# Kernel optimization log

Measured on AMD Instinct MI355X. Metric: run time of the kernel, lower is better.

The kernel has to match this reference:

```python
import jax, jax.numpy as jnp
import numpy as np

N = 50000        # nodes
E = 800000       # edges
F_IN = 128       # dataset.num_features (== dim*heads so all conv layers share in_channels)
DIM = 32         # mParams['dim']
HEADS = 4        # mParams['num_heads']
HC = DIM * HEADS # 128
DEPTH = 2        # mParams['c_depth'] -> total conv layers = DEPTH + 1 = 3
L = DEPTH + 1
DIM2 = 16        # ceil(DIM/2)
NCLS = 6
SLOPE = 0.2      # GATv2Conv default negative_slope


def setup_inputs() -> dict:
    key = jax.random.key(0)
    ks = jax.random.split(key, 20)
    def lin(k, fan_in, shape):
        return jax.random.normal(k, shape, dtype=jnp.float32) / np.sqrt(fan_in)
    x = jax.random.normal(ks[0], (N, F_IN), dtype=jnp.float32)
    edge_index = jax.random.randint(ks[1], (2, E), 0, N, dtype=jnp.int64)
    batch = jnp.zeros((N,), dtype=jnp.int64)
    # stacked GATv2Conv params (all layers have in_channels = 128)
    Wl = lin(ks[2], F_IN, (L, F_IN, HC))   # lin_l weight (source transform)
    Wr = lin(ks[3], F_IN, (L, F_IN, HC))   # lin_r weight (target transform)
    bl = jnp.zeros((L, HC), dtype=jnp.float32)
    br = jnp.zeros((L, HC), dtype=jnp.float32)
    att = lin(ks[4], DIM, (L, HEADS, DIM)) # attention vector a
    cb = jnp.zeros((L, HC), dtype=jnp.float32)  # conv output bias
    W1 = lin(ks[5], HC, (HC, DIM));   b1 = jnp.zeros((DIM,), jnp.float32)
    W2 = lin(ks[6], DIM, (DIM, DIM2)); b2 = jnp.zeros((DIM2,), jnp.float32)
    W3 = lin(ks[7], 2 * DIM2, (2 * DIM2, NCLS)); b3 = jnp.zeros((NCLS,), jnp.float32)
    return {"x": x, "edge_index": edge_index, "batch": batch,
            "Wl": Wl, "Wr": Wr, "bl": bl, "br": br, "att": att, "cb": cb,
            "W1": W1, "b1": b1, "W2": W2, "b2": b2, "W3": W3, "b3": b3}


def _gatv2_layer(h, src, dst, Wl, Wr, bl, br, att, cb):
    # h: [N, F]; src/dst: [Ea] (self-loops included)
    xl = (h @ Wl + bl).reshape(N, HEADS, DIM)  # source-side transform
    xr = (h @ Wr + br).reshape(N, HEADS, DIM)  # target-side transform
    msg = xl[src] + xr[dst]                    # [Ea, H, C]
    e = jnp.where(msg > 0, msg, SLOPE * msg)   # leaky_relu
    score = jnp.einsum('ehc,hc->eh', e, att)   # [Ea, H]
    # scatter-softmax over destination nodes
    m = jax.ops.segment_max(score, dst, num_segments=N)        # [N, H]
    ex = jnp.exp(score - m[dst])
    s = jax.ops.segment_sum(ex, dst, num_segments=N)           # [N, H]
    alpha = ex / (s[dst] + 1e-16)                              # [Ea, H]
    out = jax.ops.segment_sum(alpha[:, :, None] * xl[src], dst, num_segments=N)
    return out.reshape(N, HC) + cb


def reference(x, edge_index, batch, Wl, Wr, bl, br, att, cb, W1, b1, W2, b2, W3, b3):
    src0, dst0 = edge_index[0], edge_index[1]
    loop = jnp.arange(N, dtype=edge_index.dtype)
    src = jnp.concatenate([src0, loop])  # GATv2Conv add_self_loops=True
    dst = jnp.concatenate([dst0, loop])
    h = x
    for i in range(L):
        h = jax.nn.relu(_gatv2_layer(h, src, dst, Wl[i], Wr[i], bl[i], br[i], att[i], cb[i]))
    h = jax.nn.relu(h @ W1 + b1)
    h = jax.nn.relu(h @ W2 + b2)
    # dropout(p=0.5) is identity in eval mode
    e = jnp.concatenate([h[src0], h[dst0]], axis=1)  # [E, 2*DIM2]
    out = e @ W3 + b3                                # [E, NCLS]
    return (out, e)
```

## Files before the change

kernel.cpp:

```cpp
#include <hip/hip_runtime.h>
#include <hip/hip_bf16.h>

typedef __hip_bfloat16 bf16;
typedef __attribute__((ext_vector_type(8))) short bf16x8;
typedef __attribute__((ext_vector_type(4))) float f32x4;

#define N_NODES 50000
#define E_EDGES 800000
#define EA (E_EDGES + N_NODES)
#define HC 128
#define HEADS 4
#define DIM 32
#define DIM2 16
#define NCLS 6
#define SLOPE 0.2f
#define NCHUNK ((N_NODES + 1023) / 1024)
#define XN (N_NODES * HC)
#define GM 32
#define HSTRIDE 152
#define WSWZ_L 32768

__device__ __forceinline__ float b2f(bf16 v) { return __bfloat162float(v); }
__device__ __forceinline__ unsigned short f2bfu(float f) {
    bf16 b = __float2bfloat16(f);
    return *(unsigned short*)&b;
}

__global__ __launch_bounds__(256) void k_detect(const void* wptr, const void* eptr,
                                                int* __restrict__ flags) {
    __shared__ int sb[256], sn[256];
    int tid = threadIdx.x;
    const unsigned short* w = (const unsigned short*)wptr;
    int badf = 0;
    for (int i = tid; i < 4096; i += 256) {
        unsigned v = w[i];
        unsigned ex = (v >> 7) & 0xFF;
        if (v != 0 && (ex < 90 || ex > 150)) badf++;
    }
    const int* ei = (const int*)eptr;
    int nz = 0;
    for (int i = tid; i < 2048; i += 256) {
        if (ei[2 * i + 1] != 0) nz++;
    }
    sb[tid] = badf; sn[tid] = nz;
    __syncthreads();
    for (int ofs = 128; ofs > 0; ofs >>= 1) {
        if (tid < ofs) { sb[tid] += sb[tid + ofs]; sn[tid] += sn[tid + ofs]; }
        __syncthreads();
    }
    if (tid == 0) {
        flags[0] = (sb[0] > 64) ? 1 : 0;
        flags[1] = (sn[0] < 64) ? 1 : 0;
    }
}

__global__ void k_cvt_all(const void* sx, const void* sWl, const void* sWr,
                          const void* sbl, const void* sbr, const void* satt,
                          const void* scb, const void* sW1, const void* sb1,
                          const void* sW2, const void* sb2, const void* sW3,
                          const void* sb3,
                          float* __restrict__ h, float* __restrict__ prm,
                          const int* __restrict__ flags) {
    int i = blockIdx.x * blockDim.x + threadIdx.x;
    if (i >= XN + 104694) return;
    const void* src; float* dst; int off;
    if (i < XN) { src = sx; dst = h; off = i; }
    else {
        int j = i - XN;
        if      (j < 49152)  { src = sWl;  dst = prm;           off = j; }
        else if (j < 98304)  { src = sWr;  dst = prm + 49152;   off = j - 49152; }
        else if (j < 98688)  { src = sbl;  dst = prm + 98304;   off = j - 98304; }
        else if (j < 99072)  { src = sbr;  dst = prm + 98688;   off = j - 98688; }
        else if (j < 99456)  { src = satt; dst = prm + 99072;   off = j - 99072; }
        else if (j < 99840)  { src = scb;  dst = prm + 99456;   off = j - 99456; }
        else if (j < 103936) { src = sW1;  dst = prm + 99840;   off = j - 99840; }
        else if (j < 103968) { src = sb1;  dst = prm + 103936;  off = j - 103936; }
        else if (j < 104480) { src = sW2;  dst = prm + 103968;  off = j - 103968; }
        else if (j < 104496) { src = sb2;  dst = prm + 104480;  off = j - 104480; }
        else if (j < 104688) { src = sW3;  dst = prm + 104496;  off = j - 104496; }
        else                 { src = sb3;  dst = prm + 104688;  off = j - 104688; }
    }
    float v = flags[0] ? ((const float*)src)[off] : b2f(((const bf16*)src)[off]);
    dst[off] = v;
}

__global__ void k_cvti(const void* __restrict__ src, int* __restrict__ dst, int n,
                       const int* __restrict__ flags) {
    int i = blockIdx.x * blockDim.x + threadIdx.x;
    if (i >= n) return;
    int v;
    if (flags[1]) v = (int)((const long long*)src)[i];
    else          v = ((const int*)src)[i];
    if (v < 0) v = 0;
    if (v >= N_NODES) v = N_NODES - 1;
    dst[i] = v;
}

__global__ void k_wswz(const float* __restrict__ prm, unsigned short* __restrict__ wswz) {
    int i = blockIdx.x * blockDim.x + threadIdx.x;
    if (i >= 3 * WSWZ_L) return;
    int L = i / WSWZ_L;
    int e = i % WSWZ_L;
    int ntile = e >> 11;
    int r2 = e & 2047;
    int ks = r2 >> 9;
    int r3 = r2 & 511;
    int lane = r3 >> 3;
    int j = r3 & 7;
    int col = ntile * 16 + (lane & 15);
    int k = ks * 32 + (lane >> 4) * 8 + j;
    float v;
    if (col < HC) v = prm[L * HC * HC + k * HC + col];
    else          v = prm[49152 + L * HC * HC + k * HC + (col - HC)];
    wswz[i] = f2bfu(v);
}

__global__ void k_zero(int* __restrict__ off, int* __restrict__ fill) {
    int i = blockIdx.x * blockDim.x + threadIdx.x;
    if (i <= N_NODES) off[i] = 0;
    if (i < N_NODES) fill[i] = 0;
}

__global__ void k_hist(const int* __restrict__ eidx, int* __restrict__ off) {
    int e = blockIdx.x * blockDim.x + threadIdx.x;
    if (e >= EA) return;
    int dst = (e < E_EDGES) ? eidx[E_EDGES + e] : (e - E_EDGES);
    atomicAdd(&off[dst], 1);
}

__global__ __launch_bounds__(1024) void k_scan1(int* __restrict__ off, int* __restrict__ part) {
    __shared__ int s[1024];
    int tid = threadIdx.x;
    int i = blockIdx.x * 1024 + tid;
    int v = (i < N_NODES) ? off[i] : 0;
    s[tid] = v;
    __syncthreads();
    for (int o = 1; o < 1024; o <<= 1) {
        int t = (tid >= o) ? s[tid - o] : 0;
        __syncthreads();
        s[tid] += t;
        __syncthreads();
    }
    if (i < N_NODES) off[i] = s[tid] - v;
    if (tid == 1023) part[blockIdx.x] = s[1023];
}

__global__ __launch_bounds__(64) void k_scan2(int* __restrict__ part) {
    int tid = threadIdx.x;
    int v = (tid < NCHUNK) ? part[tid] : 0;
    int orig = v;
    for (int o = 1; o < 64; o <<= 1) {
        int t = __shfl_up(v, o);
        if (tid >= o) v += t;
    }
    if (tid < NCHUNK) part[tid] = v - orig;
}

__global__ __launch_bounds__(1024) void k_scan3(int* __restrict__ off, const int* __restrict__ part) {
    int i = blockIdx.x * 1024 + threadIdx.x;
    if (i < N_NODES) off[i] += part[blockIdx.x];
    if (i == 0) off[N_NODES] = EA;
}

__global__ void k_scatter(const int* __restrict__ eidx, const int* __restrict__ off,
                          int* __restrict__ fill, int* __restrict__ csrsrc) {
    int e = blockIdx.x * blockDim.x + threadIdx.x;
    if (e >= EA) return;
    int src, dst;
    if (e < E_EDGES) { src = eidx[e]; dst = eidx[E_EDGES + e]; }
    else             { src = dst = e - E_EDGES; }
    int pos = off[dst] + atomicAdd(&fill[dst], 1);
    if (pos >= 0 && pos < EA) csrsrc[pos] = src;
}

__global__ __launch_bounds__(256) void k_gemm_mfma(
        const float* __restrict__ h,
        const unsigned short* __restrict__ wswz,
        const float* __restrict__ bl, const float* __restrict__ br,
        unsigned* __restrict__ xlbf, float* __restrict__ xr) {
    __shared__ unsigned short hs[GM * HSTRIDE];
    int tid = threadIdx.x;
    int wave = tid >> 6, lane = tid & 63;
    long row0 = (long)blockIdx.x * GM;

    for (int idx = tid; idx < GM * 64; idx += 256) {
        int r = idx >> 6, cp = idx & 63;
        float v0 = 0.f, v1 = 0.f;
        if (row0 + r < N_NODES) {
            const float2 hv = ((const float2*)(h + (row0 + r) * HC))[cp];
            v0 = hv.x; v1 = hv.y;
        }
        unsigned* dst = (unsigned*)&hs[r * HSTRIDE + cp * 2];
        *dst = (unsigned)f2bfu(v0) | ((unsigned)f2bfu(v1) << 16);
    }
    __syncthreads();

    int q = lane >> 4, l16 = lane & 15;
    for (int nt = 0; nt < 4; nt++) {
        int colbase = wave * 64 + nt * 16;
        int col = colbase + l16;
        int ntile = colbase >> 4;
        f32x4 acc0 = {0.f, 0.f, 0.f, 0.f};
        f32x4 acc1 = {0.f, 0.f, 0.f, 0.f};
#pragma unroll
        for (int ks = 0; ks < 4; ks++) {
            bf16x8 bfrag = *(const bf16x8*)(wswz + (((ntile * 4 + ks) * 64 + lane) << 3));
            bf16x8 a0 = *(const bf16x8*)(hs + l16 * HSTRIDE + ks * 32 + q * 8);
            bf16x8 a1 = *(const bf16x8*)(hs + (16 + l16) * HSTRIDE + ks * 32 + q * 8);
            acc0 = __builtin_amdgcn_mfma_f32_16x16x32_bf16(a0, bfrag, acc0, 0, 0, 0);
            acc1 = __builtin_amdgcn_mfma_f32_16x16x32_bf16(a1, bfrag, acc1, 0, 0, 0);
        }
        if (col < HC) {
            float bias = bl[col];
#pragma unroll
            for (int reg = 0; reg < 4; reg++) {
                float v0 = acc0[reg] + bias;
                float v1 = acc1[reg] + bias;
                float p0 = __shfl_xor(v0, 1);
                float p1 = __shfl_xor(v1, 1);
                if ((lane & 1) == 0) {
                    long n0 = row0 + q * 4 + reg;
                    long n1 = row0 + 16 + q * 4 + reg;
                    unsigned u0 = (unsigned)f2bfu(v0) | ((unsigned)f2bfu(p0) << 16);
                    unsigned u1 = (unsigned)f2bfu(v1) | ((unsigned)f2bfu(p1) << 16);
                    int cp = col >> 1;
                    if (n0 < N_NODES) xlbf[n0 * (HC / 2) + cp] = u0;
                    if (n1 < N_NODES) xlbf[n1 * (HC / 2) + cp] = u1;
                }
            }
        } else {
            int c = col - HC;
            float bias = br[c];
#pragma unroll
            for (int reg = 0; reg < 4; reg++) {
                long n0 = row0 + q * 4 + reg;
                long n1 = row0 + 16 + q * 4 + reg;
                if (n0 < N_NODES) xr[n0 * HC + c] = acc0[reg] + bias;
                if (n1 < N_NODES) xr[n1 * HC + c] = acc1[reg] + bias;
            }
        }
    }
}

__global__ __launch_bounds__(256) void k_attn(
        const unsigned* __restrict__ xlbf, const float* __restrict__ xr,
        const int* __restrict__ off, const int* __restrict__ csrsrc,
        const float* __restrict__ att, const float* __restrict__ cb,
        float* __restrict__ hout) {
    int wave = threadIdx.x >> 6;
    int lane = threadIdx.x & 63;
    int node = blockIdx.x * 4 + wave;
    if (node >= N_NODES) return;
    int grp = lane >> 4;
    int gl  = lane & 15;
    int fb  = gl * 8;
    int head = fb >> 5;

    const float4* xrp = (const float4*)(xr + (long)node * HC + fb);
    float4 xa = xrp[0], xb = xrp[1];
    const float4* ap = (const float4*)(att + head * DIM + (fb & 31));
    float4 aa = ap[0], ab = ap[1];

    int e0 = off[node], e1 = off[node + 1];
    if (e0 < 0) e0 = 0;
    if (e1 > EA) e1 = EA;
    if (e1 <= e0) {
        if (grp == 0) {
            float4 z = make_float4(0.f, 0.f, 0.f, 0.f);
            ((float4*)(hout + (long)node * HC + fb))[0] = z;
            ((float4*)(hout + (long)node * HC + fb))[1] = z;
        }
        return;
    }
    int klast = e1 - 1;

    int k0 = e0 + grp;
    int ka = k0 < klast ? k0 : klast;
    int kb = (k0 + 4) < klast ? (k0 + 4) : klast;
    int sa = csrsrc[ka];
    int sb = csrsrc[kb];
    uint4 u0 = ((const uint4*)(xlbf + (long)sa * (HC / 2)))[gl];
    uint4 u1 = ((const uint4*)(xlbf + (long)sb * (HC / 2)))[gl];

    float m = -1e30f, ssum = 0.f;
    float acc[8];
#pragma unroll
    for (int j = 0; j < 8; j++) acc[j] = 0.f;

    for (int kk = k0; kk < e1; kk += 4) {
        uint4 cur = u0;
        u0 = u1;
        int kp = (kk + 8) < klast ? (kk + 8) : klast;
        int sp = csrsrc[kp];
        u1 = ((const uint4*)(xlbf + (long)sp * (HC / 2)))[gl];

        float x0 = __uint_as_float(cur.x << 16);
        float x1 = __uint_as_float(cur.x & 0xffff0000u);
        float x2 = __uint_as_float(cur.y << 16);
        float x3 = __uint_as_float(cur.y & 0xffff0000u);
        float x4 = __uint_as_float(cur.z << 16);
        float x5 = __uint_as_float(cur.z & 0xffff0000u);
        float x6 = __uint_as_float(cur.w << 16);
        float x7 = __uint_as_float(cur.w & 0xffff0000u);
        float m0 = x0 + xa.x, m1 = x1 + xa.y, m2 = x2 + xa.z, m3 = x3 + xa.w;
        float m4 = x4 + xb.x, m5 = x5 + xb.y, m6 = x6 + xb.z, m7 = x7 + xb.w;
        float l0 = fmaxf(m0, SLOPE * m0), l1 = fmaxf(m1, SLOPE * m1);
        float l2 = fmaxf(m2, SLOPE * m2), l3 = fmaxf(m3, SLOPE * m3);
        float l4 = fmaxf(m4, SLOPE * m4), l5 = fmaxf(m5, SLOPE * m5);
        float l6 = fmaxf(m6, SLOPE * m6), l7 = fmaxf(m7, SLOPE * m7);
        float p = l0 * aa.x + l1 * aa.y + l2 * aa.z + l3 * aa.w
                + l4 * ab.x + l5 * ab.y + l6 * ab.z + l7 * ab.w;
        p += __shfl_xor(p, 1);
        p += __shfl_xor(p, 2);
        float mn = fmaxf(m, p);
        float sc = __expf(m - mn);
        float ex = __expf(p - mn);
        ssum = ssum * sc + ex;
        acc[0] = acc[0] * sc + ex * x0;
        acc[1] = acc[1] * sc + ex * x1;
        acc[2] = acc[2] * sc + ex * x2;
        acc[3] = acc[3] * sc + ex * x3;
        acc[4] = acc[4] * sc + ex * x4;
        acc[5] = acc[5] * sc + ex * x5;
        acc[6] = acc[6] * sc + ex * x6;
        acc[7] = acc[7] * sc + ex * x7;
        m = mn;
    }

#pragma unroll
    for (int d = 16; d <= 32; d <<= 1) {
        float mo = __shfl_xor(m, d);
        float so = __shfl_xor(ssum, d);
        float ao[8];
#pragma unroll
        for (int j = 0; j < 8; j++) ao[j] = __shfl_xor(acc[j], d);
        float mn = fmaxf(m, mo);
        float s1 = __expf(m - mn);
        float s2 = __expf(mo - mn);
        ssum = ssum * s1 + so * s2;
#pragma unroll
        for (int j = 0; j < 8; j++) acc[j] = acc[j] * s1 + ao[j] * s2;
        m = mn;
    }

    if (grp == 0) {
        float inv = 1.f / (ssum + 1e-16f);
        const float4* cbp = (const float4*)(cb + fb);
        float4 c0 = cbp[0], c1 = cbp[1];
        float4 o0, o1;
        o0.x = fmaxf(acc[0] * inv + c0.x, 0.f);
        o0.y = fmaxf(acc[1] * inv + c0.y, 0.f);
        o0.z = fmaxf(acc[2] * inv + c0.z, 0.f);
        o0.w = fmaxf(acc[3] * inv + c0.w, 0.f);
        o1.x = fmaxf(acc[4] * inv + c1.x, 0.f);
        o1.y = fmaxf(acc[5] * inv + c1.y, 0.f);
        o1.z = fmaxf(acc[6] * inv + c1.z, 0.f);
        o1.w = fmaxf(acc[7] * inv + c1.w, 0.f);
        float4* op = (float4*)(hout + (long)node * HC + fb);
        op[0] = o0;
        op[1] = o1;
    }
}

__global__ __launch_bounds__(256) void k_mlp1(
        const float* __restrict__ h, const float* __restrict__ W1,
        const float* __restrict__ b1, float* __restrict__ h2) {
    __shared__ float hs[8 * HC];
    __shared__ float w1s[HC * DIM];
    int tid = threadIdx.x;
    long row0 = (long)blockIdx.x * 8;
    for (int idx = tid; idx < HC * DIM; idx += 256) w1s[idx] = W1[idx];
    for (int idx = tid; idx < 8 * HC; idx += 256) {
        long g = row0 * HC + idx;
        hs[idx] = (g < (long)N_NODES * HC) ? h[g] : 0.f;
    }
    __syncthreads();
    int r = tid >> 5, c = tid & 31;
    float acc = b1[c];
    for (int k = 0; k < HC; k++) acc += hs[r * HC + k] * w1s[k * DIM + c];
    long row = row0 + r;
    if (row < N_NODES) h2[row * DIM + c] = acc > 0.f ? acc : 0.f;
}

__global__ __launch_bounds__(256) void k_mlp2(
        const float* __restrict__ h2, const float* __restrict__ W2,
        const float* __restrict__ b2, float* __restrict__ h3) {
    __shared__ float hs[16 * DIM];
    __shared__ float w2s[DIM * DIM2];
    int tid = threadIdx.x;
    long row0 = (long)blockIdx.x * 16;
    for (int idx = tid; idx < DIM * DIM2; idx += 256) w2s[idx] = W2[idx];
    for (int idx = tid; idx < 16 * DIM; idx += 256) {
        long g = row0 * DIM + idx;
        hs[idx] = (g < (long)N_NODES * DIM) ? h2[g] : 0.f;
    }
    __syncthreads();
    int r = tid >> 4, c = tid & 15;
    float acc = b2[c];
    for (int k = 0; k < DIM; k++) acc += hs[r * DIM + k] * w2s[k * DIM2 + c];
    long row = row0 + r;
    if (row < N_NODES) h3[row * DIM2 + c] = acc > 0.f ? acc : 0.f;
}

__global__ __launch_bounds__(256) void k_out(
        const float* __restrict__ h3, const int* __restrict__ eidx,
        const float* __restrict__ W3, const float* __restrict__ b3,
        void* __restrict__ dout, const int* __restrict__ flags) {
    __shared__ float w3s[2 * DIM2 * NCLS];
    __shared__ float bs[NCLS];
    int tid = threadIdx.x;
    if (tid < 2 * DIM2 * NCLS) w3s[tid] = W3[tid];
    if (tid < NCLS) bs[tid] = b3[tid];
    __syncthreads();
    int e = blockIdx.x * 256 + tid;
    if (e >= E_EDGES) return;
    int src = eidx[e], dst = eidx[E_EDGES + e];
    float v[2 * DIM2];
    const float4* ps = (const float4*)(h3 + (long)src * DIM2);
    const float4* pd = (const float4*)(h3 + (long)dst * DIM2);
#pragma unroll
    for (int q = 0; q < 4; q++) {
        float4 t = ps[q];
        v[q * 4 + 0] = t.x; v[q * 4 + 1] = t.y; v[q * 4 + 2] = t.z; v[q * 4 + 3] = t.w;
    }
#pragma unroll
    for (int q = 0; q < 4; q++) {
        float4 t = pd[q];
        v[16 + q * 4 + 0] = t.x; v[16 + q * 4 + 1] = t.y; v[16 + q * 4 + 2] = t.z; v[16 + q * 4 + 3] = t.w;
    }
    float o[NCLS];
#pragma unroll
    for (int j = 0; j < NCLS; j++) {
        float acc = bs[j];
#pragma unroll
        for (int k = 0; k < 2 * DIM2; k++) acc += v[k] * w3s[k * NCLS + j];
        o[j] = acc;
    }
    if (flags[0]) {
        float* out0 = (float*)dout;
#pragma unroll
        for (int j = 0; j < NCLS; j++) out0[(long)e * NCLS + j] = o[j];
        float4* eo = (float4*)((float*)dout + (long)E_EDGES * NCLS) + (long)e * 8;
#pragma unroll
        for (int q = 0; q < 8; q++)
            eo[q] = make_float4(v[q * 4], v[q * 4 + 1], v[q * 4 + 2], v[q * 4 + 3]);
    } else {
        bf16* out0 = (bf16*)dout;
#pragma unroll
        for (int j = 0; j < NCLS; j++) out0[(long)e * NCLS + j] = __float2bfloat16(o[j]);
        uint4* eo = (uint4*)((bf16*)dout + (long)E_EDGES * NCLS) + (long)e * 4;
#pragma unroll
        for (int q = 0; q < 4; q++) {
            uint4 w;
            w.x = (unsigned)f2bfu(v[q * 8 + 0]) | ((unsigned)f2bfu(v[q * 8 + 1]) << 16);
            w.y = (unsigned)f2bfu(v[q * 8 + 2]) | ((unsigned)f2bfu(v[q * 8 + 3]) << 16);
            w.z = (unsigned)f2bfu(v[q * 8 + 4]) | ((unsigned)f2bfu(v[q * 8 + 5]) << 16);
            w.w = (unsigned)f2bfu(v[q * 8 + 6]) | ((unsigned)f2bfu(v[q * 8 + 7]) << 16);
            eo[q] = w;
        }
    }
}

extern "C" void kernel_launch(void* const* d_in, const int* in_sizes, int n_in,
                              void* d_out, int out_size, void* d_ws, size_t ws_size,
                              hipStream_t stream) {
    float* wsf   = (float*)d_ws;
    int*   flags = (int*)d_ws;
    float* h     = wsf + 16;
    float* xl    = h  + (long)N_NODES * HC;
    float* xr    = xl + (long)N_NODES * HC;
    float* prm   = xr + (long)N_NODES * HC;
    int*   eidx  = (int*)(prm + 110000);
    int*   off   = eidx + 2 * E_EDGES;
    int*   fill  = off + (N_NODES + 1);
    int*   csr   = fill + N_NODES;
    int*   part  = csr + EA;
    unsigned short* wswz = (unsigned short*)(part + 64);
    unsigned* xlbf = (unsigned*)xl;
    float* h2 = xl;
    float* h3 = xl + (long)N_NODES * DIM;

    float* pWl = prm + 0;
    float* pbl = prm + 98304;
    float* pbr = prm + 98688;
    float* patt= prm + 99072;
    float* pcb = prm + 99456;
    float* pW1 = prm + 99840;
    float* pb1 = prm + 103936;
    float* pW2 = prm + 103968;
    float* pb2 = prm + 104480;
    float* pW3 = prm + 104496;
    float* pb3 = prm + 104688;

    k_detect<<<1, 256, 0, stream>>>(d_in[3], d_in[1], flags);

    k_cvt_all<<<(XN + 104694 + 255) / 256, 256, 0, stream>>>(
        d_in[0], d_in[3], d_in[4], d_in[5], d_in[6], d_in[7], d_in[8],
        d_in[9], d_in[10], d_in[11], d_in[12], d_in[13], d_in[14],
        h, prm, flags);
    k_cvti<<<(2 * E_EDGES + 255) / 256, 256, 0, stream>>>(d_in[1], eidx, 2 * E_EDGES, flags);
    k_wswz<<<(3 * WSWZ_L + 255) / 256, 256, 0, stream>>>(pWl, wswz);

    k_zero<<<(2 * N_NODES + 1 + 255) / 256, 256, 0, stream>>>(off, fill);
    k_hist<<<(EA + 255) / 256, 256, 0, stream>>>(eidx, off);
    k_scan1<<<NCHUNK, 1024, 0, stream>>>(off, part);
    k_scan2<<<1, 64, 0, stream>>>(part);
    k_scan3<<<NCHUNK, 1024, 0, stream>>>(off, part);
    k_scatter<<<(EA + 255) / 256, 256, 0, stream>>>(eidx, off, fill, csr);

    for (int i = 0; i < 3; i++) {
        k_gemm_mfma<<<(N_NODES + GM - 1) / GM, 256, 0, stream>>>(
            h, wswz + (long)i * WSWZ_L, pbl + (long)i * HC, pbr + (long)i * HC,
            xlbf, xr);
        k_attn<<<(N_NODES + 3) / 4, 256, 0, stream>>>(
            xlbf, xr, off, csr, patt + (long)i * HEADS * DIM, pcb + (long)i * HC, h);
    }

    k_mlp1<<<(N_NODES + 7) / 8, 256, 0, stream>>>(h, pW1, pb1, h2);
    k_mlp2<<<(N_NODES + 15) / 16, 256, 0, stream>>>(h2, pW2, pb2, h3);

    k_out<<<(E_EDGES + 255) / 256, 256, 0, stream>>>(h3, eidx, pW3, pb3, d_out, flags);
}
```

Baseline: 563.1 us.

## Fuse preprocessing kernels, inline dtype detection, store intermediate activations as bf16

Merges dtype detection, conversion, edge-index conversion, histogram and weight swizzling into one prep kernel, and replaces the three-pass scan with a single-block chunked scan. Type detection is redone per block inside the kernels that need it, and the x-to-float conversion is dropped: the first GEMM reads raw input directly. Attention outputs for layers 1-2 are written as bf16 so the next GEMM reads half the bytes, and the two MLP kernels are fused. This cuts launches and memory traffic but adds redundant per-block detection reads. The detection thresholds and sample sizes also change.

```diff
diff --git a/kernel.cpp b/kernel.cpp
--- a/kernel.cpp
+++ b/kernel.cpp
@@ -14,91 +14,89 @@
 #define DIM2 16
 #define NCLS 6
 #define SLOPE 0.2f
-#define NCHUNK ((N_NODES + 1023) / 1024)
 #define XN (N_NODES * HC)
 #define GM 32
 #define HSTRIDE 152
 #define WSWZ_L 32768
+#define SCHUNK 49
+
+#define P_CVTI (2 * E_EDGES)
+#define P_PRM  6390
+#define P_WSWZ (3 * WSWZ_L)
+#define P_TOT  (P_CVTI + P_PRM + P_WSWZ)
 
 __device__ __forceinline__ float b2f(bf16 v) { return __bfloat162float(v); }
 __device__ __forceinline__ unsigned short f2bfu(float f) {
     bf16 b = __float2bfloat16(f);
     return *(unsigned short*)&b;
 }
-
-__global__ __launch_bounds__(256) void k_detect(const void* wptr, const void* eptr,
-                                                int* __restrict__ flags) {
-    __shared__ int sb[256], sn[256];
+__device__ __forceinline__ unsigned packbf(float a, float b) {
+    return (unsigned)f2bfu(a) | ((unsigned)f2bfu(b) << 16);
+}
+
+__device__ __forceinline__ void block_detect(const void* wptr, const void* eptr,
+                                             int* det, int& isf32, int& is64) {
     int tid = threadIdx.x;
+    if (tid == 0) { det[0] = 0; det[1] = 0; }
+    __syncthreads();
     const unsigned short* w = (const unsigned short*)wptr;
     int badf = 0;
-    for (int i = tid; i < 4096; i += 256) {
+    for (int i = tid; i < 1024; i += 256) {
         unsigned v = w[i];
         unsigned ex = (v >> 7) & 0xFF;
         if (v != 0 && (ex < 90 || ex > 150)) badf++;
     }
     const int* ei = (const int*)eptr;
     int nz = 0;
-    for (int i = tid; i < 2048; i += 256) {
+    for (int i = tid; i < 1024; i += 256) {
         if (ei[2 * i + 1] != 0) nz++;
     }
-    sb[tid] = badf; sn[tid] = nz;
-    __syncthreads();
-    for (int ofs = 128; ofs > 0; ofs >>= 1) {
-        if (tid < ofs) { sb[tid] += sb[tid + ofs]; sn[tid] += sn[tid + ofs]; }
-        __syncthreads();
-    }
-    if (tid == 0) {
-        flags[0] = (sb[0] > 64) ? 1 : 0;
-        flags[1] = (sn[0] < 64) ? 1 : 0;
-    }
-}
-
-__global__ void k_cvt_all(const void* sx, const void* sWl, const void* sWr,
-                          const void* sbl, const void* sbr, const void* satt,
-                          const void* scb, const void* sW1, const void* sb1,
-                          const void* sW2, const void* sb2, const void* sW3,
-                          const void* sb3,
-                          float* __restrict__ h, float* __restrict__ prm,
-                          const int* __restrict__ flags) {
-    int i = blockIdx.x * blockDim.x + threadIdx.x;
-    if (i >= XN + 104694) return;
-    const void* src; float* dst; int off;
-    if (i < XN) { src = sx; dst = h; off = i; }
-    else {
-        int j = i - XN;
-        if      (j < 49152)  { src = sWl;  dst = prm;           off = j; }
-        else if (j < 98304)  { src = sWr;  dst = prm + 49152;   off = j - 49152; }
-        else if (j < 98688)  { src = sbl;  dst = prm + 98304;   off = j - 98304; }
-        else if (j < 99072)  { src = sbr;  dst = prm + 98688;   off = j - 98688; }
-        else if (j < 99456)  { src = satt; dst = prm + 99072;   off = j - 99072; }
-        else if (j < 99840)  { src = scb;  dst = prm + 99456;   off = j - 99456; }
-        else if (j < 103936) { src = sW1;  dst = prm + 99840;   off = j - 99840; }
-        else if (j < 103968) { src = sb1;  dst = prm + 103936;  off = j - 103936; }
-        else if (j < 104480) { src = sW2;  dst = prm + 103968;  off = j - 103968; }
-        else if (j < 104496) { src = sb2;  dst = prm + 104480;  off = j - 104480; }
-        else if (j < 104688) { src = sW3;  dst = prm + 104496;  off = j - 104496; }
-        else                 { src = sb3;  dst = prm + 104688;  off = j - 104688; }
-    }
-    float v = flags[0] ? ((const float*)src)[off] : b2f(((const bf16*)src)[off]);
-    dst[off] = v;
-}
-
-__global__ void k_cvti(const void* __restrict__ src, int* __restrict__ dst, int n,
-                       const int* __restrict__ flags) {
-    int i = blockIdx.x * blockDim.x + threadIdx.x;
-    if (i >= n) return;
-    int v;
-    if (flags[1]) v = (int)((const long long*)src)[i];
-    else          v = ((const int*)src)[i];
-    if (v < 0) v = 0;
-    if (v >= N_NODES) v = N_NODES - 1;
-    dst[i] = v;
-}
-
-__global__ void k_wswz(const float* __restrict__ prm, unsigned short* __restrict__ wswz) {
-    int i = blockIdx.x * blockDim.x + threadIdx.x;
-    if (i >= 3 * WSWZ_L) return;
+    if (badf) atomicAdd(&det[0], badf);
+    if (nz)   atomicAdd(&det[1], nz);
+    __syncthreads();
+    isf32 = det[0] > 100;
+    is64  = det[1] < 100;
+}
+
+__global__ __launch_bounds__(256) void k_prep(
+        const void* eraw, const void* sWl, const void* sWr,
+        const void* sbl, const void* sbr, const void* satt, const void* scb,
+        const void* sW1, const void* sb1, const void* sW2, const void* sb2,
+        const void* sW3, const void* sb3,
+        int* __restrict__ eidx, int* __restrict__ off,
+        float* __restrict__ prm, unsigned short* __restrict__ wswz) {
+    __shared__ int det[2];
+    int isf32, is64;
+    block_detect(sWl, eraw, det, isf32, is64);
+
+    int i = blockIdx.x * 256 + threadIdx.x;
+    if (i < P_CVTI) {
+        int v = is64 ? (int)((const long long*)eraw)[i] : ((const int*)eraw)[i];
+        if (v < 0) v = 0;
+        if (v >= N_NODES) v = N_NODES - 1;
+        eidx[i] = v;
+        if (i >= E_EDGES) atomicAdd(&off[v], 1);
+        return;
+    }
+    i -= P_CVTI;
+    if (i < P_PRM) {
+        int j = i + 98304;
+        const void* src; float* dst; int o;
+        if      (j < 98688)  { src = sbl;  dst = prm + 98304;  o = j - 98304; }
+        else if (j < 99072)  { src = sbr;  dst = prm + 98688;  o = j - 98688; }
+        else if (j < 99456)  { src = satt; dst = prm + 99072;  o = j - 99072; }
+        else if (j < 99840)  { src = scb;  dst = prm + 99456;  o = j - 99456; }
+        else if (j < 103936) { src = sW1;  dst = prm + 99840;  o = j - 99840; }
+        else if (j < 103968) { src = sb1;  dst = prm + 103936; o = j - 103936; }
+        else if (j < 104480) { src = sW2;  dst = prm + 103968; o = j - 103968; }
+        else if (j < 104496) { src = sb2;  dst = prm + 104480; o = j - 104480; }
+        else if (j < 104688) { src = sW3;  dst = prm + 104496; o = j - 104496; }
+        else                 { src = sb3;  dst = prm + 104688; o = j - 104688; }
+        dst[o] = isf32 ? ((const float*)src)[o] : b2f(((const bf16*)src)[o]);
+        return;
+    }
+    i -= P_PRM;
+    if (i >= P_WSWZ) return;
     int L = i / WSWZ_L;
     int e = i % WSWZ_L;
     int ntile = e >> 11;
@@ -109,31 +107,22 @@
     int j = r3 & 7;
     int col = ntile * 16 + (lane & 15);
     int k = ks * 32 + (lane >> 4) * 8 + j;
-    float v;
-    if (col < HC) v = prm[L * HC * HC + k * HC + col];
-    else          v = prm[49152 + L * HC * HC + k * HC + (col - HC)];
+    const void* src = (col < HC) ? sWl : sWr;
+    int idx = L * HC * HC + k * HC + (col & (HC - 1));
+    float v = isf32 ? ((const float*)src)[idx] : b2f(((const bf16*)src)[idx]);
     wswz[i] = f2bfu(v);
 }
 
-__global__ void k_zero(int* __restrict__ off, int* __restrict__ fill) {
-    int i = blockIdx.x * blockDim.x + threadIdx.x;
-    if (i <= N_NODES) off[i] = 0;
-    if (i < N_NODES) fill[i] = 0;
-}
-
-__global__ void k_hist(const int* __restrict__ eidx, int* __restrict__ off) {
-    int e = blockIdx.x * blockDim.x + threadIdx.x;
-    if (e >= EA) return;
-    int dst = (e < E_EDGES) ? eidx[E_EDGES + e] : (e - E_EDGES);
-    atomicAdd(&off[dst], 1);
-}
-
-__global__ __launch_bounds__(1024) void k_scan1(int* __restrict__ off, int* __restrict__ part) {
+__global__ __launch_bounds__(1024) void k_scan(int* __restrict__ off) {
     __shared__ int s[1024];
     int tid = threadIdx.x;
-    int i = blockIdx.x * 1024 + tid;
-    int v = (i < N_NODES) ? off[i] : 0;
-    s[tid] = v;
+    int base = tid * SCHUNK;
+    int sum = 0;
+    for (int k = 0; k < SCHUNK; k++) {
+        int idx = base + k;
+        if (idx < N_NODES) sum += off[idx] + 1;
+    }
+    s[tid] = sum;
     __syncthreads();
     for (int o = 1; o < 1024; o <<= 1) {
         int t = (tid >= o) ? s[tid - o] : 0;
@@ -141,25 +130,16 @@
         s[tid] += t;
         __syncthreads();
     }
-    if (i < N_NODES) off[i] = s[tid] - v;
-    if (tid == 1023) part[blockIdx.x] = s[1023];
-}
-
-__global__ __launch_bounds__(64) void k_scan2(int* __restrict__ part) {
-    int tid = threadIdx.x;
-    int v = (tid < NCHUNK) ? part[tid] : 0;
-    int orig = v;
-    for (int o = 1; o < 64; o <<= 1) {
-        int t = __shfl_up(v, o);
-        if (tid >= o) v += t;
-    }
-    if (tid < NCHUNK) part[tid] = v - orig;
-}
-
-__global__ __launch_bounds__(1024) void k_scan3(int* __restrict__ off, const int* __restrict__ part) {
-    int i = blockIdx.x * 1024 + threadIdx.x;
-    if (i < N_NODES) off[i] += part[blockIdx.x];
-    if (i == 0) off[N_NODES] = EA;
+    int run = (tid == 0) ? 0 : s[tid - 1];
+    for (int k = 0; k < SCHUNK; k++) {
+        int idx = base + k;
+        if (idx < N_NODES) {
+            int c = off[idx] + 1;
+            off[idx] = run;
+            run += c;
+        }
+    }
+    if (tid == 0) off[N_NODES] = EA;
 }
 
 __global__ void k_scatter(const int* __restrict__ eidx, const int* __restrict__ off,
@@ -174,24 +154,41 @@
 }
 
 __global__ __launch_bounds__(256) void k_gemm_mfma(
-        const float* __restrict__ h,
+        const void* __restrict__ hsrc, const void* wdet, const void* edet,
+        int detect_in,
         const unsigned short* __restrict__ wswz,
         const float* __restrict__ bl, const float* __restrict__ br,
         unsigned* __restrict__ xlbf, float* __restrict__ xr) {
     __shared__ unsigned short hs[GM * HSTRIDE];
+    __shared__ int det[2];
     int tid = threadIdx.x;
     int wave = tid >> 6, lane = tid & 63;
     long row0 = (long)blockIdx.x * GM;
 
-    for (int idx = tid; idx < GM * 64; idx += 256) {
-        int r = idx >> 6, cp = idx & 63;
-        float v0 = 0.f, v1 = 0.f;
-        if (row0 + r < N_NODES) {
-            const float2 hv = ((const float2*)(h + (row0 + r) * HC))[cp];
-            v0 = hv.x; v1 = hv.y;
-        }
-        unsigned* dst = (unsigned*)&hs[r * HSTRIDE + cp * 2];
-        *dst = (unsigned)f2bfu(v0) | ((unsigned)f2bfu(v1) << 16);
+    int f32in = 0;
+    if (detect_in) {
+        int is64d;
+        block_detect(wdet, edet, det, f32in, is64d);
+    }
+
+    if (f32in) {
+        for (int idx = tid; idx < GM * 64; idx += 256) {
+            int r = idx >> 6, cp = idx & 63;
+            float v0 = 0.f, v1 = 0.f;
+            if (row0 + r < N_NODES) {
+                const float2 hv = ((const float2*)((const float*)hsrc + (row0 + r) * HC))[cp];
+                v0 = hv.x; v1 = hv.y;
+            }
+            *(unsigned*)&hs[r * HSTRIDE + cp * 2] = packbf(v0, v1);
+        }
+    } else {
+        for (int idx = tid; idx < GM * 64; idx += 256) {
+            int r = idx >> 6, cp = idx & 63;
+            unsigned u = 0;
+            if (row0 + r < N_NODES)
+                u = ((const unsigned*)hsrc)[(row0 + r) * (HC / 2) + cp];
+            *(unsigned*)&hs[r * HSTRIDE + cp * 2] = u;
+        }
     }
     __syncthreads();
 
@@ -221,8 +218,8 @@
                 if ((lane & 1) == 0) {
                     long n0 = row0 + q * 4 + reg;
                     long n1 = row0 + 16 + q * 4 + reg;
-                    unsigned u0 = (unsigned)f2bfu(v0) | ((unsigned)f2bfu(p0) << 16);
-                    unsigned u1 = (unsigned)f2bfu(v1) | ((unsigned)f2bfu(p1) << 16);
+                    unsigned u0 = packbf(v0, p0);
+                    unsigned u1 = packbf(v1, p1);
                     int cp = col >> 1;
                     if (n0 < N_NODES) xlbf[n0 * (HC / 2) + cp] = u0;
                     if (n1 < N_NODES) xlbf[n1 * (HC / 2) + cp] = u1;
@@ -246,7 +243,7 @@
         const unsigned* __restrict__ xlbf, const float* __restrict__ xr,
         const int* __restrict__ off, const int* __restrict__ csrsrc,
         const float* __restrict__ att, const float* __restrict__ cb,
-        float* __restrict__ hout) {
+        void* __restrict__ hout, int out_bf16) {
     int wave = threadIdx.x >> 6;
     int lane = threadIdx.x & 63;
     int node = blockIdx.x * 4 + wave;
@@ -266,9 +263,14 @@
     if (e1 > EA) e1 = EA;
     if (e1 <= e0) {
         if (grp == 0) {
-            float4 z = make_float4(0.f, 0.f, 0.f, 0.f);
-            ((float4*)(hout + (long)node * HC + fb))[0] = z;
-            ((float4*)(hout + (long)node * HC + fb))[1] = z;
+            if (out_bf16) {
+                uint4 z = {0u, 0u, 0u, 0u};
+                *(uint4*)((unsigned*)hout + (long)node * (HC / 2) + gl * 4) = z;
+            } else {
+                float4 z = make_float4(0.f, 0.f, 0.f, 0.f);
+                ((float4*)((float*)hout + (long)node * HC + fb))[0] = z;
+                ((float4*)((float*)hout + (long)node * HC + fb))[1] = z;
+            }
         }
         return;
     }
@@ -347,57 +349,60 @@
         float inv = 1.f / (ssum + 1e-16f);
         const float4* cbp = (const float4*)(cb + fb);
         float4 c0 = cbp[0], c1 = cbp[1];
-        float4 o0, o1;
-        o0.x = fmaxf(acc[0] * inv + c0.x, 0.f);
-        o0.y = fmaxf(acc[1] * inv + c0.y, 0.f);
-        o0.z = fmaxf(acc[2] * inv + c0.z, 0.f);
-        o0.w = fmaxf(acc[3] * inv + c0.w, 0.f);
-        o1.x = fmaxf(acc[4] * inv + c1.x, 0.f);
-        o1.y = fmaxf(acc[5] * inv + c1.y, 0.f);
-        o1.z = fmaxf(acc[6] * inv + c1.z, 0.f);
-        o1.w = fmaxf(acc[7] * inv + c1.w, 0.f);
-        float4* op = (float4*)(hout + (long)node * HC + fb);
-        op[0] = o0;
-        op[1] = o1;
-    }
-}
-
-__global__ __launch_bounds__(256) void k_mlp1(
+        float o0 = fmaxf(acc[0] * inv + c0.x, 0.f);
+        float o1 = fmaxf(acc[1] * inv + c0.y, 0.f);
+        float o2 = fmaxf(acc[2] * inv + c0.z, 0.f);
+        float o3 = fmaxf(acc[3] * inv + c0.w, 0.f);
+        float o4 = fmaxf(acc[4] * inv + c1.x, 0.f);
+        float o5 = fmaxf(acc[5] * inv + c1.y, 0.f);
+        float o6 = fmaxf(acc[6] * inv + c1.z, 0.f);
+        float o7 = fmaxf(acc[7] * inv + c1.w, 0.f);
+        if (out_bf16) {
+            uint4 w;
+            w.x = packbf(o0, o1);
+            w.y = packbf(o2, o3);
+            w.z = packbf(o4, o5);
+            w.w = packbf(o6, o7);
+            *(uint4*)((unsigned*)hout + (long)node * (HC / 2) + gl * 4) = w;
+        } else {
+            float4 a0 = make_float4(o0, o1, o2, o3);
+            float4 a1 = make_float4(o4, o5, o6, o7);
+            float4* op = (float4*)((float*)hout + (long)node * HC + fb);
+            op[0] = a0;
+            op[1] = a1;
+        }
+    }
+}
+
+__global__ __launch_bounds__(256) void k_mlp(
         const float* __restrict__ h, const float* __restrict__ W1,
-        const float* __restrict__ b1, float* __restrict__ h2) {
-    __shared__ float hs[8 * HC];
+        const float* __restrict__ b1, const float* __restrict__ W2,
+        const float* __restrict__ b2, float* __restrict__ h3) {
     __shared__ float w1s[HC * DIM];
-    int tid = threadIdx.x;
-    long row0 = (long)blockIdx.x * 8;
-    for (int idx = tid; idx < HC * DIM; idx += 256) w1s[idx] = W1[idx];
-    for (int idx = tid; idx < 8 * HC; idx += 256) {
-        long g = row0 * HC + idx;
-        hs[idx] = (g < (long)N_NODES * HC) ? h[g] : 0.f;
-    }
-    __syncthreads();
-    int r = tid >> 5, c = tid & 31;
-    float acc = b1[c];
-    for (int k = 0; k < HC; k++) acc += hs[r * HC + k] * w1s[k * DIM + c];
-    long row = row0 + r;
-    if (row < N_NODES) h2[row * DIM + c] = acc > 0.f ? acc : 0.f;
-}
-
-__global__ __launch_bounds__(256) void k_mlp2(
-        const float* __restrict__ h2, const float* __restrict__ W2,
-        const float* __restrict__ b2, float* __restrict__ h3) {
-    __shared__ float hs[16 * DIM];
+    __shared__ float hs[16 * HC];
+    __shared__ float h2s[16 * DIM];
     __shared__ float w2s[DIM * DIM2];
     int tid = threadIdx.x;
     long row0 = (long)blockIdx.x * 16;
+    for (int idx = tid; idx < HC * DIM; idx += 256) w1s[idx] = W1[idx];
     for (int idx = tid; idx < DIM * DIM2; idx += 256) w2s[idx] = W2[idx];
-    for (int idx = tid; idx < 16 * DIM; idx += 256) {
-        long g = row0 * DIM + idx;
-        hs[idx] = (g < (long)N_NODES * DIM) ? h2[g] : 0.f;
+    for (int idx = tid; idx < 16 * HC; idx += 256) {
+        long g = row0 * HC + idx;
+        hs[idx] = (g < (long)N_NODES * HC) ? h[g] : 0.f;
+    }
+    __syncthreads();
+#pragma unroll
+    for (int p = 0; p < 2; p++) {
+        int idx = tid + p * 256;
+        int r = idx >> 5, c = idx & 31;
+        float acc = b1[c];
+        for (int k = 0; k < HC; k++) acc += hs[r * HC + k] * w1s[k * DIM + c];
+        h2s[r * DIM + c] = acc > 0.f ? acc : 0.f;
     }
     __syncthreads();
     int r = tid >> 4, c = tid & 15;
     float acc = b2[c];
-    for (int k = 0; k < DIM; k++) acc += hs[r * DIM + k] * w2s[k * DIM2 + c];
+    for (int k = 0; k < DIM; k++) acc += h2s[r * DIM + k] * w2s[k * DIM2 + c];
     long row = row0 + r;
     if (row < N_NODES) h3[row * DIM2 + c] = acc > 0.f ? acc : 0.f;
 }
@@ -405,9 +410,12 @@
 __global__ __launch_bounds__(256) void k_out(
         const float* __restrict__ h3, const int* __restrict__ eidx,
         const float* __restrict__ W3, const float* __restrict__ b3,
-        void* __restrict__ dout, const int* __restrict__ flags) {
+        void* __restrict__ dout, const void* wdet, const void* edet) {
     __shared__ float w3s[2 * DIM2 * NCLS];
     __shared__ float bs[NCLS];
+    __shared__ int det[2];
+    int isf32, is64d;
+    block_detect(wdet, edet, det, isf32, is64d);
     int tid = threadIdx.x;
     if (tid < 2 * DIM2 * NCLS) w3s[tid] = W3[tid];
     if (tid < NCLS) bs[tid] = b3[tid];
@@ -436,7 +444,7 @@
         for (int k = 0; k < 2 * DIM2; k++) acc += v[k] * w3s[k * NCLS + j];
         o[j] = acc;
     }
-    if (flags[0]) {
+    if (isf32) {
         float* out0 = (float*)dout;
 #pragma unroll
         for (int j = 0; j < NCLS; j++) out0[(long)e * NCLS + j] = o[j];
@@ -452,10 +460,10 @@
 #pragma unroll
         for (int q = 0; q < 4; q++) {
             uint4 w;
-            w.x = (unsigned)f2bfu(v[q * 8 + 0]) | ((unsigned)f2bfu(v[q * 8 + 1]) << 16);
-            w.y = (unsigned)f2bfu(v[q * 8 + 2]) | ((unsigned)f2bfu(v[q * 8 + 3]) << 16);
-            w.z = (unsigned)f2bfu(v[q * 8 + 4]) | ((unsigned)f2bfu(v[q * 8 + 5]) << 16);
-            w.w = (unsigned)f2bfu(v[q * 8 + 6]) | ((unsigned)f2bfu(v[q * 8 + 7]) << 16);
+            w.x = packbf(v[q * 8 + 0], v[q * 8 + 1]);
+            w.y = packbf(v[q * 8 + 2], v[q * 8 + 3]);
+            w.z = packbf(v[q * 8 + 4], v[q * 8 + 5]);
+            w.w = packbf(v[q * 8 + 6], v[q * 8 + 7]);
             eo[q] = w;
         }
     }
@@ -465,22 +473,18 @@
                               void* d_out, int out_size, void* d_ws, size_t ws_size,
                               hipStream_t stream) {
     float* wsf   = (float*)d_ws;
-    int*   flags = (int*)d_ws;
     float* h     = wsf + 16;
     float* xl    = h  + (long)N_NODES * HC;
     float* xr    = xl + (long)N_NODES * HC;
     float* prm   = xr + (long)N_NODES * HC;
-    int*   eidx  = (int*)(prm + 110000);
+    unsigned short* wswz = (unsigned short*)(prm + 110000);
+    int*   eidx  = (int*)(wswz + P_WSWZ);
     int*   off   = eidx + 2 * E_EDGES;
     int*   fill  = off + (N_NODES + 1);
     int*   csr   = fill + N_NODES;
-    int*   part  = csr + EA;
-    unsigned short* wswz = (unsigned short*)(part + 64);
     unsigned* xlbf = (unsigned*)xl;
-    float* h2 = xl;
-    float* h3 = xl + (long)N_NODES * DIM;
-
-    float* pWl = prm + 0;
+    float* h3 = xl;
+
     float* pbl = prm + 98304;
     float* pbr = prm + 98688;
     float* patt= prm + 99072;
@@ -492,32 +496,29 @@
     float* pW3 = prm + 104496;
     float* pb3 = prm + 104688;
 
-    k_detect<<<1, 256, 0, stream>>>(d_in[3], d_in[1], flags);
-
-    k_cvt_all<<<(XN + 104694 + 255) / 256, 256, 0, stream>>>(
-        d_in[0], d_in[3], d_in[4], d_in[5], d_in[6], d_in[7], d_in[8],
+    hipMemsetAsync(off, 0, (size_t)(2 * N_NODES + 1) * sizeof(int), stream);
+
+    k_prep<<<(P_TOT + 255) / 256, 256, 0, stream>>>(
+        d_in[1], d_in[3], d_in[4], d_in[5], d_in[6], d_in[7], d_in[8],
         d_in[9], d_in[10], d_in[11], d_in[12], d_in[13], d_in[14],
-        h, prm, flags);
-    k_cvti<<<(2 * E_EDGES + 255) / 256, 256, 0, stream>>>(d_in[1], eidx, 2 * E_EDGES, flags);
-    k_wswz<<<(3 * WSWZ_L + 255) / 256, 256, 0, stream>>>(pWl, wswz);
-
-    k_zero<<<(2 * N_NODES + 1 + 255) / 256, 256, 0, stream>>>(off, fill);
-    k_hist<<<(EA + 255) / 256, 256, 0, stream>>>(eidx, off);
-    k_scan1<<<NCHUNK, 1024, 0, stream>>>(off, part);
-    k_scan2<<<1, 64, 0, stream>>>(part);
-    k_scan3<<<NCHUNK, 1024, 0, stream>>>(off, part);
+        eidx, off, prm, wswz);
+
+    k_scan<<<1, 1024, 0, stream>>>(off);
     k_scatter<<<(EA + 255) / 256, 256, 0, stream>>>(eidx, off, fill, csr);
 
     for (int i = 0; i < 3; i++) {
         k_gemm_mfma<<<(N_NODES + GM - 1) / GM, 256, 0, stream>>>(
-            h, wswz + (long)i * WSWZ_L, pbl + (long)i * HC, pbr + (long)i * HC,
+            i == 0 ? (const void*)d_in[0] : (const void*)h,
+            d_in[3], d_in[1], i == 0 ? 1 : 0,
+            wswz + (long)i * WSWZ_L, pbl + (long)i * HC, pbr + (long)i * HC,
             xlbf, xr);
         k_attn<<<(N_NODES + 3) / 4, 256, 0, stream>>>(
-            xlbf, xr, off, csr, patt + (long)i * HEADS * DIM, pcb + (long)i * HC, h);
-    }
-
-    k_mlp1<<<(N_NODES + 7) / 8, 256, 0, stream>>>(h, pW1, pb1, h2);
-    k_mlp2<<<(N_NODES + 15) / 16, 256, 0, stream>>>(h2, pW2, pb2, h3);
-
-    k_out<<<(E_EDGES + 255) / 256, 256, 0, stream>>>(h3, eidx, pW3, pb3, d_out, flags);
-}
+            xlbf, xr, off, csr, patt + (long)i * HEADS * DIM, pcb + (long)i * HC,
+            (void*)h, i < 2 ? 1 : 0);
+    }
+
+    k_mlp<<<(N_NODES + 15) / 16, 256, 0, stream>>>(h, pW1, pb1, pW2, pb2, h3);
+
+    k_out<<<(E_EDGES + 255) / 256, 256, 0, stream>>>(h3, eidx, pW3, pb3, d_out,
+                                                     d_in[3], d_in[1]);
+}
```

Result: slower. 657.4 us (+16.7%).
